# Kernel tuning notes

Hardware: AMD Instinct MI355X
Metric: run time of the kernel (lower is better)

## Reference

```python
import jax, jax.numpy as jnp
import numpy as np
import math

EMBED_DIM = 16
H = 4
HEAD = EMBED_DIM // H
REL_MAX = 64
M_STEPS = 8
L = 500000


def _to_c(x):
    # x: [..., 2] (real, imag) -> complex
    return x[..., 0] + 1j * x[..., 1]


def _to_r(z):
    return jnp.stack([jnp.real(z), jnp.imag(z)], axis=-1)


def setup_inputs() -> dict:
    key = jax.random.key(0)
    ks = jax.random.split(key, 12)
    s = 1.0 / math.sqrt(2 * EMBED_DIM)
    return {
        'candidate': jax.random.normal(ks[0], (EMBED_DIM, 2), jnp.float32),
        'z_past': jax.random.normal(ks[1], (L, EMBED_DIM, 2), jnp.float32),
        'q_w': jax.random.normal(ks[2], (32, 32), jnp.float32) * s,
        'q_b': jax.random.normal(ks[3], (32,), jnp.float32) * s,
        'k_w': jax.random.normal(ks[4], (32, 32), jnp.float32) * s,
        'k_b': jax.random.normal(ks[5], (32,), jnp.float32) * s,
        'v_w': jax.random.normal(ks[6], (32, 32), jnp.float32) * s,
        'v_b': jax.random.normal(ks[7], (32,), jnp.float32) * s,
        'o_w': jax.random.normal(ks[8], (32, 32), jnp.float32) * s,
        'o_b': jax.random.normal(ks[9], (32,), jnp.float32) * s,
        'rel_bias': jax.random.normal(ks[10], (2 * REL_MAX + 1, EMBED_DIM, 2), jnp.float32) * 0.02,
        'coupling': jnp.float32(0.12),
        'norm_scale': jnp.float32(1.0),
        'pos': L,
    }


def _layer_norm(x, eps=1e-5):
    m = jnp.mean(x, axis=-1, keepdims=True)
    v = jnp.mean((x - m) ** 2, axis=-1, keepdims=True)
    return (x - m) / jnp.sqrt(v + eps)


def _mish(x):
    return x * jnp.tanh(jax.nn.softplus(x))


def reference(candidate, z_past, q_w, q_b, k_w, k_b, v_w, v_b, o_w, o_b,
              rel_bias, coupling, norm_scale, pos):
    Lp = z_past.shape[0]
    # k/v projections are independent of the recurrent state -> hoist out of loop
    kv_in = z_past.reshape(Lp, 2 * EMBED_DIM)  # interleaved (r,i) like view_as_real().flatten(-2)
    k_c = _to_c((kv_in @ k_w.T + k_b).reshape(Lp, EMBED_DIM, 2)).reshape(Lp, H, HEAD)
    v_c = _to_c((kv_in @ v_w.T + v_b).reshape(Lp, EMBED_DIM, 2)).reshape(Lp, H, HEAD)
    idx = jnp.clip(jnp.arange(pos - Lp, pos) + REL_MAX, 0, 2 * REL_MAX)
    bias_h = _to_c(rel_bias)[idx].reshape(Lp, H, HEAD)
    inv_sqrt_d = 1.0 / math.sqrt(HEAD)

    z = _to_c(candidate)  # [EMBED_DIM] complex
    for _ in range(M_STEPS):
        q_r = _to_r(z).reshape(2 * EMBED_DIM)
        q_c = _to_c((q_r @ q_w.T + q_b).reshape(EMBED_DIM, 2)).reshape(H, HEAD)
        dot = jnp.real(jnp.sum(jnp.conj(q_c)[None] * k_c, axis=-1))      # [L, H]
        rel = jnp.real(jnp.sum(jnp.conj(q_c)[None] * bias_h, axis=-1))   # [L, H]
        w = jax.nn.softmax((dot + rel) * inv_sqrt_d, axis=0)             # over past_len
        out_h = jnp.sum(w[..., None] * v_c, axis=0).reshape(EMBED_DIM)
        out_r = _to_r(out_h).reshape(2 * EMBED_DIM)
        mod = _to_c((out_r @ o_w.T + o_b).reshape(EMBED_DIM, 2))
        z = z + coupling * mod
        z = _mish(jnp.real(z)) + 1j * _mish(jnp.imag(z))
        z = (_layer_norm(jnp.real(z)) + 1j * _layer_norm(jnp.imag(z))) * norm_scale
    return _to_r(z)  # [EMBED_DIM, 2]
```

## Files before the change

kernel.cpp:

```cpp
#include <hip/hip_runtime.h>

#define NB 256
#define BT 512
#define MSTEPS 8
#define CHUNK 1954
#define LDSR 1120

typedef float v8f __attribute__((ext_vector_type(8)));
typedef float v4f __attribute__((ext_vector_type(4)));


struct PParams {
  const float* candidate;
  const float* z_past;
  const float* q_w; const float* q_b;
  const float* k_w; const float* k_b;
  const float* v_w; const float* v_b;
  const float* o_w; const float* o_b;
  const float* rel_bias;
  const float* coupling;
  const float* norm_scale;
  float* out;
  float* ws;
  int L;
};

__device__ __forceinline__ float mish_f(float x) {
  float sp = fmaxf(x, 0.0f) + log1pf(expf(-fabsf(x)));
  return x * tanhf(sp);
}

__device__ void compute_qar(const PParams& p, int tid,
                            float* sZ, float* sQ, float* sA, float* sRel) {
  if (tid < 32) {
    float acc = p.q_b[tid];
    const float* row = p.q_w + tid * 32;
    #pragma unroll
    for (int c = 0; c < 32; ++c) acc = fmaf(row[c], sZ[c], acc);
    sQ[tid] = acc;
  }
  __syncthreads();
  if (tid < 128) {
    int h = tid >> 5, c = tid & 31;
    float acc = 0.f;
    #pragma unroll
    for (int jj = 0; jj < 8; ++jj)
      acc = fmaf(sQ[8 * h + jj], p.k_w[(8 * h + jj) * 32 + c], acc);
    sA[tid] = 0.5f * acc;
  }
  if (tid >= 256) {
    int t = tid - 256;
    int l = t >> 2, h = t & 3;
    float acc = 0.f;
    #pragma unroll
    for (int jj = 0; jj < 8; ++jj) {
      int jidx = 8 * h + jj;
      acc = fmaf(sQ[jidx],
                 p.rel_bias[(l + 64) * 32 + jidx] - p.rel_bias[128 * 32 + jidx],
                 acc);
    }
    sRel[t] = 0.5f * acc;
  }
  __syncthreads();
}

__device__ __forceinline__ void trip_body(const v8f (&A)[4], v8f zv,
                                          const float* sRel, bool dorel, int relrow,
                                          v8f (&S)[4], v4f& Zc) {
  float d0 = 0.f, d1 = 0.f, d2 = 0.f, d3 = 0.f;
  #pragma unroll
  for (int k = 0; k < 8; ++k) {
    d0 = fmaf(A[0][k], zv[k], d0);
    d1 = fmaf(A[1][k], zv[k], d1);
    d2 = fmaf(A[2][k], zv[k], d2);
    d3 = fmaf(A[3][k], zv[k], d3);
  }
  d0 += __shfl_xor(d0, 1); d0 += __shfl_xor(d0, 2);
  d1 += __shfl_xor(d1, 1); d1 += __shfl_xor(d1, 2);
  d2 += __shfl_xor(d2, 1); d2 += __shfl_xor(d2, 2);
  d3 += __shfl_xor(d3, 1); d3 += __shfl_xor(d3, 2);
  if (dorel) {
    const float4 r = reinterpret_cast<const float4*>(sRel)[relrow];
    d0 += r.x; d1 += r.y; d2 += r.z; d3 += r.w;
  }
  float w0 = __expf(d0), w1 = __expf(d1), w2 = __expf(d2), w3 = __expf(d3);
  Zc[0] += w0; Zc[1] += w1; Zc[2] += w2; Zc[3] += w3;
  S[0] += zv * w0;
  S[1] += zv * w1;
  S[2] += zv * w2;
  S[3] += zv * w3;
}

__global__ __launch_bounds__(BT)
void photonic_kernel(PParams p) {
  __shared__ float sZ[32];
  __shared__ float sQ[32];
  __shared__ float sOutV[32];
  __shared__ float sZn[32];
  __shared__ __align__(16) float sA[128];
  __shared__ __align__(16) float sRel[256];
  __shared__ float sRed[BT / 64][4][36];
  __shared__ float sP[132][4];
  __shared__ float sSS[128];
  __shared__ float sSZ[4];
  __shared__ __align__(16) float sZp[LDSR * 32];

  const int tid  = threadIdx.x;
  const int b    = blockIdx.x;
  const int j    = tid & 3;
  const int quad = tid >> 2;
  const int wave = tid >> 6;
  const int lane = tid & 63;

  const int chunk0 = b * CHUNK;
  const int clen   = min(CHUNK, p.L - chunk0);
  const int ldsl   = min(clen, (int)LDSR);

  if (tid < 32) sZ[tid] = p.candidate[tid];
  __syncthreads();
  compute_qar(p, tid, sZ, sQ, sA, sRel);

  for (int iter = 0; iter < MSTEPS; ++iter) {
    v8f A[4];
    #pragma unroll
    for (int h = 0; h < 4; ++h)
      A[h] = *reinterpret_cast<const v8f*>(sA + h * 32 + j * 8);

    v8f S[4];
    #pragma unroll
    for (int h = 0; h < 4; ++h) S[h] = 0.f;
    v4f Zc = 0.f;

    if (iter == 0) {
      #pragma unroll
      for (int t = 0; t < 9; ++t) {
        int li = quad + (t << 7);
        if (li < ldsl) {
          v8f zv = *reinterpret_cast<const v8f*>(
              p.z_past + (size_t)(chunk0 + li) * 32 + j * 8);
          float* dst = sZp + li * 32 + j * 8;
          *reinterpret_cast<v4f*>(dst)     = __builtin_shufflevector(zv, zv, 0, 1, 2, 3);
          *reinterpret_cast<v4f*>(dst + 4) = __builtin_shufflevector(zv, zv, 4, 5, 6, 7);
          trip_body(A, zv, sRel, (b == 0) && (t == 0) && (quad < 64), quad, S, Zc);
        }
      }
    } else {
      #pragma unroll
      for (int t = 0; t < 9; ++t) {
        int li = quad + (t << 7);
        if (li < ldsl) {
          const float* src = sZp + li * 32 + j * 8;
          v4f a4 = *reinterpret_cast<const v4f*>(src);
          v4f b4 = *reinterpret_cast<const v4f*>(src + 4);
          v8f zv = __builtin_shufflevector(a4, b4, 0, 1, 2, 3, 4, 5, 6, 7);
          trip_body(A, zv, sRel, (b == 0) && (t == 0) && (quad < 64), quad, S, Zc);
        }
      }
    }
    for (int r = LDSR + quad; r < clen; r += 128) {
      v8f zv = *reinterpret_cast<const v8f*>(
          p.z_past + (size_t)(chunk0 + r) * 32 + j * 8);
      trip_body(A, zv, sRel, false, 0, S, Zc);
    }

    #pragma unroll
    for (int m = 4; m <= 32; m <<= 1) {
      #pragma unroll
      for (int h = 0; h < 4; ++h) {
        #pragma unroll
        for (int k = 0; k < 8; ++k) S[h][k] += __shfl_xor(S[h][k], m);
        Zc[h] += __shfl_xor(Zc[h], m);
      }
    }
    if ((lane >> 2) == 0) {
      #pragma unroll
      for (int h = 0; h < 4; ++h) {
        #pragma unroll
        for (int k = 0; k < 8; ++k) sRed[wave][lane][h * 8 + k] = S[h][k];
        sRed[wave][lane][32 + h] = Zc[h];
      }
    }
    __syncthreads();

    float* pb = p.ws + 1280 + iter * (132 * NB);
    if (tid < 132) {
      float acc = 0.f;
      if (tid < 128) {
        int h = tid >> 5, c = tid & 31;
        int jj = c >> 3, k = c & 7;
        #pragma unroll
        for (int w2 = 0; w2 < BT / 64; ++w2) acc += sRed[w2][jj][h * 8 + k];
      } else {
        int h = tid - 128;
        #pragma unroll
        for (int w2 = 0; w2 < BT / 64; ++w2) acc += sRed[w2][0][32 + h];
      }
      __hip_atomic_store(&pb[tid * NB + b], acc, __ATOMIC_RELAXED,
                         __HIP_MEMORY_SCOPE_SYSTEM);
    }
    asm volatile("s_waitcnt vmcnt(0)" ::: "memory");
    __syncthreads();

    {
      unsigned* cbase = reinterpret_cast<unsigned*>(p.ws) + iter * 160;
      if (tid == 0) {
        unsigned* sub = cbase + ((b >> 5) << 4);
        unsigned* sup = cbase + 128;
        unsigned* flg = cbase + 144;
        if (__hip_atomic_fetch_add(sub, 1u, __ATOMIC_RELAXED,
                                   __HIP_MEMORY_SCOPE_SYSTEM) == 31u) {
          if (__hip_atomic_fetch_add(sup, 1u, __ATOMIC_RELAXED,
                                     __HIP_MEMORY_SCOPE_SYSTEM) == 7u) {
            __hip_atomic_store(flg, 1u, __ATOMIC_RELAXED,
                               __HIP_MEMORY_SCOPE_SYSTEM);
          }
        }
        while (__hip_atomic_load(flg, __ATOMIC_RELAXED,
                                 __HIP_MEMORY_SCOPE_SYSTEM) == 0u)
          __builtin_amdgcn_s_sleep(1);
      }
      __syncthreads();
    }

    {
      const int cc = tid >> 2;
      const int qq = tid & 3;
      const float4* pp =
          reinterpret_cast<const float4*>(pb + cc * NB) + qq * (NB / 16);
      float acc = 0.f;
      #pragma unroll
      for (int i = 0; i < NB / 16; ++i) {
        float4 v4 = pp[i];
        acc += (v4.x + v4.y) + (v4.z + v4.w);
      }
      sP[cc][qq] = acc;
      if (tid < 16) {
        const int cc2 = 128 + (tid >> 2);
        const float4* pp2 =
            reinterpret_cast<const float4*>(pb + cc2 * NB) + qq * (NB / 16);
        float acc2 = 0.f;
        #pragma unroll
        for (int i = 0; i < NB / 16; ++i) {
          float4 v4 = pp2[i];
          acc2 += (v4.x + v4.y) + (v4.z + v4.w);
        }
        sP[cc2][qq] = acc2;
      }
    }
    __syncthreads();
    if (tid < 132) {
      float acc = sP[tid][0] + sP[tid][1] + sP[tid][2] + sP[tid][3];
      if (tid < 128) sSS[tid] = acc; else sSZ[tid - 128] = acc;
    }
    __syncthreads();

    if (tid < 32) {
      int h = tid >> 3;
      float acc = 0.f;
      const float* row = p.v_w + tid * 32;
      #pragma unroll
      for (int c = 0; c < 32; ++c) acc = fmaf(row[c], sSS[h * 32 + c], acc);
      sOutV[tid] = acc / sSZ[h] + p.v_b[tid];
    }
    __syncthreads();
    if (tid < 32) {
      float acc = p.o_b[tid];
      const float* row = p.o_w + tid * 32;
      #pragma unroll
      for (int c = 0; c < 32; ++c) acc = fmaf(row[c], sOutV[c], acc);
      float zv2 = sZ[tid] + p.coupling[0] * acc;
      sZn[tid] = mish_f(zv2);
    }
    __syncthreads();
    if (tid < 32) {
      int par = tid & 1;
      float m = 0.f;
      #pragma unroll
      for (int e = 0; e < 16; ++e) m += sZn[2 * e + par];
      m *= (1.f / 16.f);
      float v = 0.f;
      #pragma unroll
      for (int e = 0; e < 16; ++e) { float dd = sZn[2 * e + par] - m; v = fmaf(dd, dd, v); }
      v *= (1.f / 16.f);
      sZ[tid] = (sZn[tid] - m) * rsqrtf(v + 1e-5f) * p.norm_scale[0];
    }
    __syncthreads();

    if (iter != MSTEPS - 1) {
      compute_qar(p, tid, sZ, sQ, sA, sRel);
    } else {
      if (b == 0 && tid < 32) p.out[tid] = sZ[tid];
    }
  }
}

extern "C" void kernel_launch(void* const* d_in, const int* in_sizes, int n_in,
                              void* d_out, int out_size, void* d_ws, size_t ws_size,
                              hipStream_t stream) {
  PParams p;
  p.candidate  = (const float*)d_in[0];
  p.z_past     = (const float*)d_in[1];
  p.q_w = (const float*)d_in[2];  p.q_b = (const float*)d_in[3];
  p.k_w = (const float*)d_in[4];  p.k_b = (const float*)d_in[5];
  p.v_w = (const float*)d_in[6];  p.v_b = (const float*)d_in[7];
  p.o_w = (const float*)d_in[8];  p.o_b = (const float*)d_in[9];
  p.rel_bias   = (const float*)d_in[10];
  p.coupling   = (const float*)d_in[11];
  p.norm_scale = (const float*)d_in[12];
  p.out = (float*)d_out;
  p.ws  = (float*)d_ws;
  p.L   = in_sizes[1] / 32;

  hipMemsetAsync(d_ws, 0, 5120, stream);

  void* args[] = { &p };
  hipLaunchCooperativeKernel((const void*)photonic_kernel,
                             dim3(NB), dim3(BT), args, 0, stream);
}
```

Baseline: 321.7 us.

## Double threads per block and split each row across eight lanes

Raises the block size from 512 to 1024 threads, so each z_past row is now handled by 8 lanes with float4 loads instead of 4 lanes with 8-float vectors. Adds one more shuffle stage to the dot-product reduction and reshapes the cross-wave reduction buffer to match. The LDS-resident portion drops to 1024 rows, with the li < ldsl guards removed, and the workspace offset is enlarged. More threads give more memory-level parallelism and shorter per-thread chains, at the cost of extra shuffles and a heavier __syncthreads. The unguarded LDS loop assumes every chunk, including the last one, has at least 1024 rows.

```diff
diff --git a/kernel.cpp b/kernel.cpp
--- a/kernel.cpp
+++ b/kernel.cpp
@@ -1,12 +1,11 @@
 #include <hip/hip_runtime.h>
 
 #define NB 256
-#define BT 512
+#define BT 1024
 #define MSTEPS 8
 #define CHUNK 1954
-#define LDSR 1120
-
-typedef float v8f __attribute__((ext_vector_type(8)));
+#define LDSR 1024
+
 typedef float v4f __attribute__((ext_vector_type(4)));
 
 
@@ -48,7 +47,7 @@
       acc = fmaf(sQ[8 * h + jj], p.k_w[(8 * h + jj) * 32 + c], acc);
     sA[tid] = 0.5f * acc;
   }
-  if (tid >= 256) {
+  if (tid >= 256 && tid < 512) {
     int t = tid - 256;
     int l = t >> 2, h = t & 3;
     float acc = 0.f;
@@ -64,21 +63,21 @@
   __syncthreads();
 }
 
-__device__ __forceinline__ void trip_body(const v8f (&A)[4], v8f zv,
+__device__ __forceinline__ void trip_body(const v4f (&A)[4], v4f zv,
                                           const float* sRel, bool dorel, int relrow,
-                                          v8f (&S)[4], v4f& Zc) {
+                                          v4f (&S)[4], v4f& Zc) {
   float d0 = 0.f, d1 = 0.f, d2 = 0.f, d3 = 0.f;
   #pragma unroll
-  for (int k = 0; k < 8; ++k) {
+  for (int k = 0; k < 4; ++k) {
     d0 = fmaf(A[0][k], zv[k], d0);
     d1 = fmaf(A[1][k], zv[k], d1);
     d2 = fmaf(A[2][k], zv[k], d2);
     d3 = fmaf(A[3][k], zv[k], d3);
   }
-  d0 += __shfl_xor(d0, 1); d0 += __shfl_xor(d0, 2);
-  d1 += __shfl_xor(d1, 1); d1 += __shfl_xor(d1, 2);
-  d2 += __shfl_xor(d2, 1); d2 += __shfl_xor(d2, 2);
-  d3 += __shfl_xor(d3, 1); d3 += __shfl_xor(d3, 2);
+  d0 += __shfl_xor(d0, 1); d0 += __shfl_xor(d0, 2); d0 += __shfl_xor(d0, 4);
+  d1 += __shfl_xor(d1, 1); d1 += __shfl_xor(d1, 2); d1 += __shfl_xor(d1, 4);
+  d2 += __shfl_xor(d2, 1); d2 += __shfl_xor(d2, 2); d2 += __shfl_xor(d2, 4);
+  d3 += __shfl_xor(d3, 1); d3 += __shfl_xor(d3, 2); d3 += __shfl_xor(d3, 4);
   if (dorel) {
     const float4 r = reinterpret_cast<const float4*>(sRel)[relrow];
     d0 += r.x; d1 += r.y; d2 += r.z; d3 += r.w;
@@ -99,7 +98,7 @@
   __shared__ float sZn[32];
   __shared__ __align__(16) float sA[128];
   __shared__ __align__(16) float sRel[256];
-  __shared__ float sRed[BT / 64][4][36];
+  __shared__ float sRed[BT / 64][8][20];
   __shared__ float sP[132][4];
   __shared__ float sSS[128];
   __shared__ float sSZ[4];
@@ -107,8 +106,8 @@
 
   const int tid  = threadIdx.x;
   const int b    = blockIdx.x;
-  const int j    = tid & 3;
-  const int quad = tid >> 2;
+  const int o    = tid & 7;
+  const int oct  = tid >> 3;
   const int wave = tid >> 6;
   const int lane = tid & 63;
 
@@ -121,79 +120,70 @@
   compute_qar(p, tid, sZ, sQ, sA, sRel);
 
   for (int iter = 0; iter < MSTEPS; ++iter) {
-    v8f A[4];
+    v4f A[4];
     #pragma unroll
     for (int h = 0; h < 4; ++h)
-      A[h] = *reinterpret_cast<const v8f*>(sA + h * 32 + j * 8);
-
-    v8f S[4];
+      A[h] = *reinterpret_cast<const v4f*>(sA + h * 32 + o * 4);
+
+    v4f S[4];
     #pragma unroll
     for (int h = 0; h < 4; ++h) S[h] = 0.f;
     v4f Zc = 0.f;
 
     if (iter == 0) {
       #pragma unroll
-      for (int t = 0; t < 9; ++t) {
-        int li = quad + (t << 7);
-        if (li < ldsl) {
-          v8f zv = *reinterpret_cast<const v8f*>(
-              p.z_past + (size_t)(chunk0 + li) * 32 + j * 8);
-          float* dst = sZp + li * 32 + j * 8;
-          *reinterpret_cast<v4f*>(dst)     = __builtin_shufflevector(zv, zv, 0, 1, 2, 3);
-          *reinterpret_cast<v4f*>(dst + 4) = __builtin_shufflevector(zv, zv, 4, 5, 6, 7);
-          trip_body(A, zv, sRel, (b == 0) && (t == 0) && (quad < 64), quad, S, Zc);
-        }
+      for (int t = 0; t < 8; ++t) {
+        int li = oct + (t << 7);
+        v4f zv = *reinterpret_cast<const v4f*>(
+            p.z_past + (size_t)(chunk0 + li) * 32 + o * 4);
+        *reinterpret_cast<v4f*>(sZp + li * 32 + o * 4) = zv;
+        trip_body(A, zv, sRel, (b == 0) && (t == 0) && (oct < 64), oct, S, Zc);
       }
     } else {
       #pragma unroll
-      for (int t = 0; t < 9; ++t) {
-        int li = quad + (t << 7);
-        if (li < ldsl) {
-          const float* src = sZp + li * 32 + j * 8;
-          v4f a4 = *reinterpret_cast<const v4f*>(src);
-          v4f b4 = *reinterpret_cast<const v4f*>(src + 4);
-          v8f zv = __builtin_shufflevector(a4, b4, 0, 1, 2, 3, 4, 5, 6, 7);
-          trip_body(A, zv, sRel, (b == 0) && (t == 0) && (quad < 64), quad, S, Zc);
-        }
-      }
-    }
-    for (int r = LDSR + quad; r < clen; r += 128) {
-      v8f zv = *reinterpret_cast<const v8f*>(
-          p.z_past + (size_t)(chunk0 + r) * 32 + j * 8);
+      for (int t = 0; t < 8; ++t) {
+        int li = oct + (t << 7);
+        v4f zv = *reinterpret_cast<const v4f*>(sZp + li * 32 + o * 4);
+        trip_body(A, zv, sRel, (b == 0) && (t == 0) && (oct < 64), oct, S, Zc);
+      }
+    }
+    for (int r = LDSR + oct; r < clen; r += 128) {
+      v4f zv = *reinterpret_cast<const v4f*>(
+          p.z_past + (size_t)(chunk0 + r) * 32 + o * 4);
       trip_body(A, zv, sRel, false, 0, S, Zc);
     }
 
     #pragma unroll
-    for (int m = 4; m <= 32; m <<= 1) {
+    for (int m = 8; m <= 32; m <<= 1) {
       #pragma unroll
       for (int h = 0; h < 4; ++h) {
         #pragma unroll
-        for (int k = 0; k < 8; ++k) S[h][k] += __shfl_xor(S[h][k], m);
+        for (int k = 0; k < 4; ++k) S[h][k] += __shfl_xor(S[h][k], m);
         Zc[h] += __shfl_xor(Zc[h], m);
       }
     }
-    if ((lane >> 2) == 0) {
+    if (lane < 8) {
       #pragma unroll
       for (int h = 0; h < 4; ++h) {
         #pragma unroll
-        for (int k = 0; k < 8; ++k) sRed[wave][lane][h * 8 + k] = S[h][k];
-        sRed[wave][lane][32 + h] = Zc[h];
-      }
-    }
-    __syncthreads();
-
-    float* pb = p.ws + 1280 + iter * (132 * NB);
+        for (int k = 0; k < 4; ++k) sRed[wave][lane][h * 4 + k] = S[h][k];
+        sRed[wave][lane][16 + h] = Zc[h];
+      }
+    }
+    __syncthreads();
+
+    float* pb = p.ws + 4096 + iter * (132 * NB);
     if (tid < 132) {
       float acc = 0.f;
       if (tid < 128) {
         int h = tid >> 5, c = tid & 31;
-        int jj = c >> 3, k = c & 7;
-        #pragma unroll
-        for (int w2 = 0; w2 < BT / 64; ++w2) acc += sRed[w2][jj][h * 8 + k];
+        int jj = c >> 2, k = c & 3;
+        #pragma unroll
+        for (int w2 = 0; w2 < BT / 64; ++w2) acc += sRed[w2][jj][h * 4 + k];
       } else {
         int h = tid - 128;
         #pragma unroll
-        for (int w2 = 0; w2 < BT / 64; ++w2) acc += sRed[w2][0][32 + h];
+        for (int w2 = 0; w2 < BT / 64; ++w2) acc += sRed[w2][0][16 + h];
       }
       __hip_atomic_store(&pb[tid * NB + b], acc, __ATOMIC_RELAXED,
                          __HIP_MEMORY_SCOPE_SYSTEM);
@@ -202,27 +192,25 @@
     __syncthreads();
 
     {
-      unsigned* cbase = reinterpret_cast<unsigned*>(p.ws) + iter * 160;
+      unsigned* cb = reinterpret_cast<unsigned*>(p.ws) + iter * 160;
       if (tid == 0) {
-        unsigned* sub = cbase + ((b >> 5) << 4);
-        unsigned* sup = cbase + 128;
-        unsigned* flg = cbase + 144;
+        unsigned* sub = cb + ((b >> 5) << 4);
         if (__hip_atomic_fetch_add(sub, 1u, __ATOMIC_RELAXED,
                                    __HIP_MEMORY_SCOPE_SYSTEM) == 31u) {
-          if (__hip_atomic_fetch_add(sup, 1u, __ATOMIC_RELAXED,
+          if (__hip_atomic_fetch_add(cb + 128, 1u, __ATOMIC_RELAXED,
                                      __HIP_MEMORY_SCOPE_SYSTEM) == 7u) {
-            __hip_atomic_store(flg, 1u, __ATOMIC_RELAXED,
+            __hip_atomic_store(cb + 144, 1u, __ATOMIC_RELAXED,
                                __HIP_MEMORY_SCOPE_SYSTEM);
           }
         }
-        while (__hip_atomic_load(flg, __ATOMIC_RELAXED,
+        while (__hip_atomic_load(cb + 144, __ATOMIC_RELAXED,
                                  __HIP_MEMORY_SCOPE_SYSTEM) == 0u)
           __builtin_amdgcn_s_sleep(1);
       }
       __syncthreads();
     }
 
-    {
+    if (tid < 512) {
       const int cc = tid >> 2;
       const int qq = tid & 3;
       const float4* pp =
```

Result: slower. 456.0 us (+41.7%).

## Replace hierarchical atomic-counter grid barrier with per-block flags and master gather

Applied to the files above, without the earlier changes.

The grid barrier now has each block write its own flag, padded to a separate cache line. Block 0 polls all 256 flags in parallel and then sets a release flag, replacing the two-level fetch_add counter tree. The LDS layout for cached z_past rows also gets an XOR swizzle on the 8-float segment index to reduce bank conflicts. The workspace grows, so the memset covers about 128KB instead of 5KB, which adds to launch cost, and block 0 adds a serial gather step on the barrier's critical path.

```diff
diff --git a/kernel.cpp b/kernel.cpp
--- a/kernel.cpp
+++ b/kernel.cpp
@@ -116,6 +116,8 @@
   const int clen   = min(CHUNK, p.L - chunk0);
   const int ldsl   = min(clen, (int)LDSR);
 
+  unsigned* uws = reinterpret_cast<unsigned*>(p.ws);
+
   if (tid < 32) sZ[tid] = p.candidate[tid];
   __syncthreads();
   compute_qar(p, tid, sZ, sQ, sA, sRel);
@@ -138,7 +140,8 @@
         if (li < ldsl) {
           v8f zv = *reinterpret_cast<const v8f*>(
               p.z_past + (size_t)(chunk0 + li) * 32 + j * 8);
-          float* dst = sZp + li * 32 + j * 8;
+          int jx = j ^ (li & 3);
+          float* dst = sZp + li * 32 + jx * 8;
           *reinterpret_cast<v4f*>(dst)     = __builtin_shufflevector(zv, zv, 0, 1, 2, 3);
           *reinterpret_cast<v4f*>(dst + 4) = __builtin_shufflevector(zv, zv, 4, 5, 6, 7);
           trip_body(A, zv, sRel, (b == 0) && (t == 0) && (quad < 64), quad, S, Zc);
@@ -149,7 +152,8 @@
       for (int t = 0; t < 9; ++t) {
         int li = quad + (t << 7);
         if (li < ldsl) {
-          const float* src = sZp + li * 32 + j * 8;
+          int jx = j ^ (li & 3);
+          const float* src = sZp + li * 32 + jx * 8;
           v4f a4 = *reinterpret_cast<const v4f*>(src);
           v4f b4 = *reinterpret_cast<const v4f*>(src + 4);
           v8f zv = __builtin_shufflevector(a4, b4, 0, 1, 2, 3, 4, 5, 6, 7);
@@ -182,7 +186,7 @@
     }
     __syncthreads();
 
-    float* pb = p.ws + 1280 + iter * (132 * NB);
+    float* pb = p.ws + 40960 + iter * (132 * NB);
     if (tid < 132) {
       float acc = 0.f;
       if (tid < 128) {
@@ -201,21 +205,21 @@
     asm volatile("s_waitcnt vmcnt(0)" ::: "memory");
     __syncthreads();
 
-    {
-      unsigned* cbase = reinterpret_cast<unsigned*>(p.ws) + iter * 160;
+    if (tid == 0)
+      __hip_atomic_store(&uws[iter * 4096 + b * 16], 1u, __ATOMIC_RELAXED,
+                         __HIP_MEMORY_SCOPE_SYSTEM);
+    if (b == 0) {
+      if (tid < NB) {
+        while (__hip_atomic_load(&uws[iter * 4096 + tid * 16], __ATOMIC_RELAXED,
+                                 __HIP_MEMORY_SCOPE_SYSTEM) == 0u) {}
+      }
+      __syncthreads();
+      if (tid == 0)
+        __hip_atomic_store(&uws[32768 + iter * 16], 1u, __ATOMIC_RELAXED,
+                           __HIP_MEMORY_SCOPE_SYSTEM);
+    } else {
       if (tid == 0) {
-        unsigned* sub = cbase + ((b >> 5) << 4);
-        unsigned* sup = cbase + 128;
-        unsigned* flg = cbase + 144;
-        if (__hip_atomic_fetch_add(sub, 1u, __ATOMIC_RELAXED,
-                                   __HIP_MEMORY_SCOPE_SYSTEM) == 31u) {
-          if (__hip_atomic_fetch_add(sup, 1u, __ATOMIC_RELAXED,
-                                     __HIP_MEMORY_SCOPE_SYSTEM) == 7u) {
-            __hip_atomic_store(flg, 1u, __ATOMIC_RELAXED,
-                               __HIP_MEMORY_SCOPE_SYSTEM);
-          }
-        }
-        while (__hip_atomic_load(flg, __ATOMIC_RELAXED,
+        while (__hip_atomic_load(&uws[32768 + iter * 16], __ATOMIC_RELAXED,
                                  __HIP_MEMORY_SCOPE_SYSTEM) == 0u)
           __builtin_amdgcn_s_sleep(1);
       }
@@ -311,7 +315,7 @@
   p.ws  = (float*)d_ws;
   p.L   = in_sizes[1] / 32;
 
-  hipMemsetAsync(d_ws, 0, 5120, stream);
+  hipMemsetAsync(d_ws, 0, 131584, stream);
 
   void* args[] = { &p };
   hipLaunchCooperativeKernel((const void*)photonic_kernel,
```

Result: faster. 305.5 us (-5.0%).
